# Kernel tuning notes

Measured on AMD Instinct MI355X. Metric: run time of the kernel, lower is better.

The kernel has to match this reference:

```python
import jax, jax.numpy as jnp
import numpy as np

MU = 5
ITERATIONS = 3


def _sobel(x):
    # torch kernel: stack([K, K.T]) with K = vertical-gradient Sobel; conv2d is cross-correlation
    k = jnp.array([[-1., -2., -1.], [0., 0., 0.], [1., 2., 1.]], dtype=x.dtype)
    kern = jnp.stack([k, k.T])[:, None]  # [2,1,3,3] -> channels (Gy, Gx)
    return jax.lax.conv_general_dilated(
        x, kern, window_strides=(1, 1), padding=[(1, 1), (1, 1)],
        dimension_numbers=("NCHW", "OIHW", "NCHW"))


def _normalize(v):
    # norm over channel dim, zeros replaced by 1 (matches tang_mag[tang_mag==0]=1)
    mag = jnp.linalg.norm(v, axis=1, keepdims=True)
    mag = jnp.where(mag == 0, jnp.ones_like(mag), mag)
    return v / mag


def etf_forward(inputs, mu=MU, iterations=ITERATIONS):
    B, _, H, W = inputs.shape
    sobel = _sobel(inputs)                                   # [B,2,H,W]
    sobel_mag = jnp.linalg.norm(sobel, axis=1, keepdims=True)
    sobel_mag = sobel_mag / jnp.max(sobel_mag)               # [B,1,H,W]
    pad = lambda t: jnp.pad(t, ((0, 0), (0, 0), (mu, mu), (mu, mu)))
    sobel_mag_padded = pad(sobel_mag)
    sobel_X = sobel_mag
    # tang = sobel.flip(channels) * [-1, 1] => [-Gx, Gy], then normalized
    tang = jnp.stack([-sobel[:, 1], sobel[:, 0]], axis=1)
    tang = _normalize(tang)
    for _ in range(iterations):
        for ori in ("Vertical", "Horizontal"):
            tang_padded = pad(tang)
            tang_X = tang
            acc = jnp.zeros_like(tang)
            for i in range(2 * mu + 1):
                if ori == "Vertical":
                    tang_Y = tang_padded[:, :, i:i + H, mu:mu + W]
                    sobel_Y = sobel_mag_padded[:, :, i:i + H, mu:mu + W]
                else:
                    tang_Y = tang_padded[:, :, mu:mu + H, i:i + W]
                    sobel_Y = sobel_mag_padded[:, :, mu:mu + H, i:i + W]
                w = (jnp.tanh(sobel_Y - sobel_X) + 1.0) * jnp.sum(tang_X * tang_Y, axis=1, keepdims=True) * 0.5
                acc = acc + tang_Y * w
            tang = _normalize(acc)
    return tang


def setup_inputs() -> dict:
    key = jax.random.key(0)
    inputs = jax.random.uniform(key, (2, 1, 1024, 1024), dtype=jnp.float32)
    return {"inputs": inputs}


def reference(inputs) -> jnp.ndarray:
    return etf_forward(inputs)
```

## Files before the change

### kernel.cpp

```cpp
#include <hip/hip_runtime.h>

#define BB 2
#define HH 1024
#define WW 1024
#define MU 5

#define TH 32
#define TW 64
#define SW (TW + 16)
#define SH (TH + 2 * MU)

__device__ __forceinline__ float fast_rcp(float x) { return __builtin_amdgcn_rcpf(x); }
__device__ __forceinline__ float fast_rsq(float x) { return __builtin_amdgcn_rsqf(x); }

#define SR 8
__global__ __launch_bounds__(256) void sobel_init(
    const float* __restrict__ x,
    float* __restrict__ tf,
    float* __restrict__ mag,
    float* __restrict__ block_max)
{
    __shared__ float xs[SR + 2][264];
    const int t = threadIdx.x;
    const int w0 = blockIdx.x * 256;
    const int h0 = blockIdx.y * SR;
    const int b = blockIdx.z;
    const size_t plane = (size_t)HH * WW;
    const float* xb = x + (size_t)b * plane;

    for (int i = t; i < (SR + 2) * 66; i += 256) {
        int r = i / 66, c4 = i % 66;
        int g = h0 - 1 + r;
        int gw = w0 - 4 + 4 * c4;
        float4 v = make_float4(0.f, 0.f, 0.f, 0.f);
        if (g >= 0 && g < HH && gw >= 0 && gw < WW)
            v = *(const float4*)(xb + (size_t)g * WW + gw);
        *(float4*)&xs[r][4 * c4] = v;
    }
    __syncthreads();

    float lmax = 0.f;
    const int c = 4 + t;
    #pragma unroll
    for (int k = 0; k < SR; ++k) {
        const float* rT = xs[k], * rM = xs[k + 1], * rB = xs[k + 2];
        float tl = rT[c - 1], tc = rT[c], tr = rT[c + 1];
        float ml = rM[c - 1],             mr = rM[c + 1];
        float bl = rB[c - 1], bc = rB[c], br = rB[c + 1];
        float s0 = (bl - tl) + 2.f * (bc - tc) + (br - tr);
        float s1 = (tr - tl) + 2.f * (mr - ml) + (br - bl);
        float m = sqrtf(fmaf(s0, s0, s1 * s1));
        float inv = (m == 0.f) ? 1.f : fast_rcp(m);
        size_t gi = (size_t)(h0 + k) * WW + (w0 + t);
        mag[(size_t)b * plane + gi] = m;
        ((float2*)tf)[(size_t)b * plane + gi] = make_float2(-s1 * inv, s0 * inv);
        lmax = fmaxf(lmax, m);
    }

    #pragma unroll
    for (int off = 32; off; off >>= 1) lmax = fmaxf(lmax, __shfl_down(lmax, off, 64));
    __shared__ float smax[4];
    if ((t & 63) == 0) smax[t >> 6] = lmax;
    __syncthreads();
    if (t == 0)
        block_max[(blockIdx.z * 128 + blockIdx.y) * 4 + blockIdx.x] =
            fmaxf(fmaxf(smax[0], smax[1]), fmaxf(smax[2], smax[3]));
}

__global__ __launch_bounds__(256) void reduce_max(
    const float* __restrict__ block_max, float* __restrict__ gmax)
{
    const int t = threadIdx.x;
    float m = 0.f;
    #pragma unroll
    for (int i = 0; i < 4; ++i) m = fmaxf(m, block_max[t + 256 * i]);
    #pragma unroll
    for (int off = 32; off; off >>= 1) m = fmaxf(m, __shfl_down(m, off, 64));
    __shared__ float smax[4];
    if ((t & 63) == 0) smax[t >> 6] = m;
    __syncthreads();
    if (t == 0) gmax[0] = fmaxf(fmaxf(smax[0], smax[1]), fmaxf(smax[2], smax[3]));
}

__global__ __launch_bounds__(256) void mag2em(
    float* __restrict__ mag, const float* __restrict__ gmax)
{
    const float s = 2.f * fast_rcp(gmax[0]);
    const int i = blockIdx.x * 256 + threadIdx.x;
    float4* p = (float4*)mag + i;
    float4 v = *p;
    v.x = __expf(-s * v.x);
    v.y = __expf(-s * v.y);
    v.z = __expf(-s * v.z);
    v.w = __expf(-s * v.w);
    *p = v;
}

template <int PLANAR_OUT>
__global__ __launch_bounds__(256) void etf_vh(
    const float* __restrict__ tin,
    float* __restrict__ tout,
    const float* __restrict__ em)
{
    __shared__ float lds[SH * SW * 3];
    float* st = lds;
    float* sm = lds + SH * SW * 2;
    float* sv = lds;

    const int t = threadIdx.x;
    const int w0 = blockIdx.x * TW;
    const int h0 = blockIdx.y * TH;
    const int b = blockIdx.z;
    const size_t plane = (size_t)HH * WW;
    const float* tb = tin + 2 * (size_t)b * plane;
    const float* mb = em + (size_t)b * plane;

    for (int i = t; i < SH * 40 + SH * 20; i += 256) {
        if (i < SH * 40) {
            int r = i / 40, c4 = i % 40;
            int g = h0 - MU + r;
            int gw = w0 - 8 + 2 * c4;
            float4 v = make_float4(0.f, 0.f, 0.f, 0.f);
            if (g >= 0 && g < HH && gw >= 0 && gw < WW)
                v = *(const float4*)(tb + 2 * ((size_t)g * WW + gw));
            *(float4*)&st[r * SW * 2 + 4 * c4] = v;
        } else {
            int j = i - SH * 40;
            int r = j / 20, c4 = j % 20;
            int g = h0 - MU + r;
            int gw = w0 - 8 + 4 * c4;
            float4 v = make_float4(1.f, 1.f, 1.f, 1.f);
            if (g >= 0 && g < HH && gw >= 0 && gw < WW)
                v = *(const float4*)(mb + (size_t)g * WW + gw);
            *(float4*)&sm[r * SW + 4 * c4] = v;
        }
    }
    __syncthreads();

    float vr0[10], vr1[10];
    #pragma unroll
    for (int k = 0; k < 10; ++k) {
        int px = t + 256 * k;
        int r = px / SW, c = px % SW;
        float2 tx = *(const float2*)&st[((r + MU) * SW + c) * 2];
        float remx = fast_rcp(sm[(r + MU) * SW + c]);
        float a0 = 0.f, a1 = 0.f;
        #pragma unroll
        for (int d = 0; d <= 2 * MU; ++d) {
            float2 ty = *(const float2*)&st[((r + d) * SW + c) * 2];
            float emy = sm[(r + d) * SW + c];
            float s = fast_rcp(fmaf(emy, remx, 1.f));
            float w = s * fmaf(tx.x, ty.x, tx.y * ty.y);
            a0 = fmaf(ty.x, w, a0);
            a1 = fmaf(ty.y, w, a1);
        }
        float n2 = fmaf(a0, a0, a1 * a1);
        float inv = (n2 == 0.f) ? 1.f : fast_rsq(n2);
        vr0[k] = a0 * inv;
        vr1[k] = a1 * inv;
    }
    __syncthreads();
    #pragma unroll
    for (int k = 0; k < 10; ++k) {
        int px = t + 256 * k;
        *(float2*)&sv[px * 2] = make_float2(vr0[k], vr1[k]);
    }
    __syncthreads();

    #pragma unroll
    for (int k = 0; k < 8; ++k) {
        int px = t + 256 * k;
        int r = px >> 6, c = px & 63;
        int sc = c + 8;
        float2 tx = *(const float2*)&sv[(r * SW + sc) * 2];
        float remx = fast_rcp(sm[(r + MU) * SW + sc]);
        float a0 = 0.f, a1 = 0.f;
        #pragma unroll
        for (int d = -MU; d <= MU; ++d) {
            float2 ty = *(const float2*)&sv[(r * SW + sc + d) * 2];
            float emy = sm[(r + MU) * SW + sc + d];
            float s = fast_rcp(fmaf(emy, remx, 1.f));
            float w = s * fmaf(tx.x, ty.x, tx.y * ty.y);
            a0 = fmaf(ty.x, w, a0);
            a1 = fmaf(ty.y, w, a1);
        }
        float n2 = fmaf(a0, a0, a1 * a1);
        float inv = (n2 == 0.f) ? 1.f : fast_rsq(n2);
        size_t gi = (size_t)(h0 + r) * WW + (w0 + c);
        if (PLANAR_OUT) {
            tout[(size_t)(2 * b)     * plane + gi] = a0 * inv;
            tout[(size_t)(2 * b + 1) * plane + gi] = a1 * inv;
        } else {
            *(float2*)&tout[2 * ((size_t)b * plane + gi)] = make_float2(a0 * inv, a1 * inv);
        }
    }
}

extern "C" void kernel_launch(void* const* d_in, const int* in_sizes, int n_in,
                              void* d_out, int out_size, void* d_ws, size_t ws_size,
                              hipStream_t stream)
{
    const float* x = (const float*)d_in[0];
    char* ws = (char*)d_ws;
    const size_t plane = (size_t)HH * WW;

    float* tfA  = (float*)ws;
    float* tfB  = (float*)(ws + sizeof(float) * BB * 2 * plane);
    float* mag  = (float*)(ws + sizeof(float) * BB * 4 * plane);
    float* gmax = (float*)(ws + sizeof(float) * BB * 6 * plane);
    float* block_max = gmax + 16;

    sobel_init<<<dim3(4, 128, BB), 256, 0, stream>>>(x, tfA, mag, block_max);
    reduce_max<<<1, 256, 0, stream>>>(block_max, gmax);
    mag2em<<<dim3(BB * plane / 1024), 256, 0, stream>>>(mag, gmax);

    dim3 g(WW / TW, HH / TH, BB);
    etf_vh<0><<<g, 256, 0, stream>>>(tfA, tfB, mag);
    etf_vh<0><<<g, 256, 0, stream>>>(tfB, tfA, mag);
    etf_vh<1><<<g, 256, 0, stream>>>(tfA, (float*)d_out, mag);
}
```

Before: 147.2 us.

## Split fused vertical-horizontal pass into register-sliding vertical and LDS horizontal kernels

Replaces the fused vertical+horizontal tile kernel, which recomputed vertical results on halo columns and staged them through LDS, with two separate kernels per iteration. The vertical kernel streams down a column strip and keeps a sliding register window of 18 rows. The horizontal kernel loads a 32x80 tile into padded LDS, and each thread keeps an 18-wide register window to produce 8 consecutive outputs. This removes the halo recompute and the LDS traffic of the fused version, at the cost of twice as many launches and an extra global round trip of the intermediate field per iteration.

```diff
diff --git a/kernel.cpp b/kernel.cpp
--- a/kernel.cpp
+++ b/kernel.cpp
@@ -5,18 +5,13 @@
 #define WW 1024
 #define MU 5
 
-#define TH 32
-#define TW 64
-#define SW (TW + 16)
-#define SH (TH + 2 * MU)
-
 __device__ __forceinline__ float fast_rcp(float x) { return __builtin_amdgcn_rcpf(x); }
 __device__ __forceinline__ float fast_rsq(float x) { return __builtin_amdgcn_rsqf(x); }
 
 #define SR 8
 __global__ __launch_bounds__(256) void sobel_init(
     const float* __restrict__ x,
-    float* __restrict__ tf,
+    float2* __restrict__ tf,
     float* __restrict__ mag,
     float* __restrict__ block_max)
 {
@@ -53,7 +48,7 @@
         float inv = (m == 0.f) ? 1.f : fast_rcp(m);
         size_t gi = (size_t)(h0 + k) * WW + (w0 + t);
         mag[(size_t)b * plane + gi] = m;
-        ((float2*)tf)[(size_t)b * plane + gi] = make_float2(-s1 * inv, s0 * inv);
+        tf[(size_t)b * plane + gi] = make_float2(-s1 * inv, s0 * inv);
         lmax = fmaxf(lmax, m);
     }
 
@@ -96,102 +91,117 @@
     *p = v;
 }
 
-template <int PLANAR_OUT>
-__global__ __launch_bounds__(256) void etf_vh(
-    const float* __restrict__ tin,
-    float* __restrict__ tout,
+#define VSTRIP 8
+__global__ __launch_bounds__(256) void etf_v(
+    const float2* __restrict__ tin, float2* __restrict__ tout,
     const float* __restrict__ em)
 {
-    __shared__ float lds[SH * SW * 3];
-    float* st = lds;
-    float* sm = lds + SH * SW * 2;
-    float* sv = lds;
-
-    const int t = threadIdx.x;
-    const int w0 = blockIdx.x * TW;
-    const int h0 = blockIdx.y * TH;
-    const int b = blockIdx.z;
-    const size_t plane = (size_t)HH * WW;
-    const float* tb = tin + 2 * (size_t)b * plane;
-    const float* mb = em + (size_t)b * plane;
-
-    for (int i = t; i < SH * 40 + SH * 20; i += 256) {
-        if (i < SH * 40) {
-            int r = i / 40, c4 = i % 40;
-            int g = h0 - MU + r;
-            int gw = w0 - 8 + 2 * c4;
-            float4 v = make_float4(0.f, 0.f, 0.f, 0.f);
-            if (g >= 0 && g < HH && gw >= 0 && gw < WW)
-                v = *(const float4*)(tb + 2 * ((size_t)g * WW + gw));
-            *(float4*)&st[r * SW * 2 + 4 * c4] = v;
-        } else {
-            int j = i - SH * 40;
-            int r = j / 20, c4 = j % 20;
-            int g = h0 - MU + r;
-            int gw = w0 - 8 + 4 * c4;
-            float4 v = make_float4(1.f, 1.f, 1.f, 1.f);
-            if (g >= 0 && g < HH && gw >= 0 && gw < WW)
-                v = *(const float4*)(mb + (size_t)g * WW + gw);
-            *(float4*)&sm[r * SW + 4 * c4] = v;
-        }
-    }
-    __syncthreads();
-
-    float vr0[10], vr1[10];
-    #pragma unroll
-    for (int k = 0; k < 10; ++k) {
-        int px = t + 256 * k;
-        int r = px / SW, c = px % SW;
-        float2 tx = *(const float2*)&st[((r + MU) * SW + c) * 2];
-        float remx = fast_rcp(sm[(r + MU) * SW + c]);
+    const int c  = blockIdx.x * 256 + threadIdx.x;
+    const int r0 = blockIdx.y * VSTRIP;
+    const int b  = blockIdx.z;
+    const size_t plane = (size_t)HH * WW;
+    const float2* tb = tin + (size_t)b * plane;
+    const float*  eb = em  + (size_t)b * plane;
+
+    float w0[VSTRIP + 10], w1[VSTRIP + 10], we[VSTRIP + 10];
+    #pragma unroll
+    for (int j = 0; j < 10; ++j) {
+        int g = r0 - MU + j;
+        float2 v = make_float2(0.f, 0.f); float e = 1.f;
+        if (g >= 0) { v = tb[(size_t)g * WW + c]; e = eb[(size_t)g * WW + c]; }
+        w0[j] = v.x; w1[j] = v.y; we[j] = e;
+    }
+    #pragma unroll
+    for (int i = 0; i < VSTRIP; ++i) {
+        int g = r0 + i + MU;
+        float2 v = make_float2(0.f, 0.f); float e = 1.f;
+        if (g < HH) { v = tb[(size_t)g * WW + c]; e = eb[(size_t)g * WW + c]; }
+        w0[i + 10] = v.x; w1[i + 10] = v.y; we[i + 10] = e;
+
+        float tx0 = w0[i + MU], tx1 = w1[i + MU];
+        float remx = fast_rcp(we[i + MU]);
         float a0 = 0.f, a1 = 0.f;
         #pragma unroll
         for (int d = 0; d <= 2 * MU; ++d) {
-            float2 ty = *(const float2*)&st[((r + d) * SW + c) * 2];
-            float emy = sm[(r + d) * SW + c];
-            float s = fast_rcp(fmaf(emy, remx, 1.f));
-            float w = s * fmaf(tx.x, ty.x, tx.y * ty.y);
-            a0 = fmaf(ty.x, w, a0);
-            a1 = fmaf(ty.y, w, a1);
+            float s = fast_rcp(fmaf(we[i + d], remx, 1.f));
+            float w = s * fmaf(tx0, w0[i + d], tx1 * w1[i + d]);
+            a0 = fmaf(w0[i + d], w, a0);
+            a1 = fmaf(w1[i + d], w, a1);
         }
         float n2 = fmaf(a0, a0, a1 * a1);
         float inv = (n2 == 0.f) ? 1.f : fast_rsq(n2);
-        vr0[k] = a0 * inv;
-        vr1[k] = a1 * inv;
-    }
-    __syncthreads();
-    #pragma unroll
-    for (int k = 0; k < 10; ++k) {
-        int px = t + 256 * k;
-        *(float2*)&sv[px * 2] = make_float2(vr0[k], vr1[k]);
-    }
-    __syncthreads();
+        tout[(size_t)b * plane + (size_t)(r0 + i) * WW + c] = make_float2(a0 * inv, a1 * inv);
+    }
+}
+
+template <int PLANAR_OUT>
+__global__ __launch_bounds__(256) void etf_h(
+    const float2* __restrict__ tin, float* __restrict__ tout,
+    const float* __restrict__ em)
+{
+    __shared__ float2 sT[32][81];
+    __shared__ float  sE[32][83];
+    const int t = threadIdx.x;
+    const int w0 = blockIdx.x * 64;
+    const int h0 = blockIdx.y * 32;
+    const int b = blockIdx.z;
+    const size_t plane = (size_t)HH * WW;
+    const float2* tb = tin + (size_t)b * plane;
+    const float*  eb = em  + (size_t)b * plane;
+
+    for (int i = t; i < 1920; i += 256) {
+        if (i < 1280) {
+            int r = i / 40, c4 = i % 40;
+            int gw = w0 - 8 + 2 * c4;
+            float4 v = make_float4(0.f, 0.f, 0.f, 0.f);
+            if (gw >= 0 && gw < WW)
+                v = *(const float4*)(tb + (size_t)(h0 + r) * WW + gw);
+            sT[r][c4 * 2]     = make_float2(v.x, v.y);
+            sT[r][c4 * 2 + 1] = make_float2(v.z, v.w);
+        } else {
+            int j = i - 1280;
+            int r = j / 20, c4 = j % 20;
+            int gw = w0 - 8 + 4 * c4;
+            float4 v = make_float4(1.f, 1.f, 1.f, 1.f);
+            if (gw >= 0 && gw < WW)
+                v = *(const float4*)(eb + (size_t)(h0 + r) * WW + gw);
+            sE[r][4 * c4] = v.x; sE[r][4 * c4 + 1] = v.y;
+            sE[r][4 * c4 + 2] = v.z; sE[r][4 * c4 + 3] = v.w;
+        }
+    }
+    __syncthreads();
+
+    const int r  = t & 31;
+    const int cg = t >> 5;
+    const int cb = 8 + cg * 8;
+    float h0a[18], h1a[18], hea[18];
+    #pragma unroll
+    for (int j = 0; j < 18; ++j) {
+        float2 v = sT[r][cb - MU + j];
+        h0a[j] = v.x; h1a[j] = v.y;
+        hea[j] = sE[r][cb - MU + j];
+    }
 
     #pragma unroll
     for (int k = 0; k < 8; ++k) {
-        int px = t + 256 * k;
-        int r = px >> 6, c = px & 63;
-        int sc = c + 8;
-        float2 tx = *(const float2*)&sv[(r * SW + sc) * 2];
-        float remx = fast_rcp(sm[(r + MU) * SW + sc]);
+        float tx0 = h0a[k + MU], tx1 = h1a[k + MU];
+        float remx = fast_rcp(hea[k + MU]);
         float a0 = 0.f, a1 = 0.f;
         #pragma unroll
-        for (int d = -MU; d <= MU; ++d) {
-            float2 ty = *(const float2*)&sv[(r * SW + sc + d) * 2];
-            float emy = sm[(r + MU) * SW + sc + d];
-            float s = fast_rcp(fmaf(emy, remx, 1.f));
-            float w = s * fmaf(tx.x, ty.x, tx.y * ty.y);
-            a0 = fmaf(ty.x, w, a0);
-            a1 = fmaf(ty.y, w, a1);
+        for (int d = 0; d <= 2 * MU; ++d) {
+            float s = fast_rcp(fmaf(hea[k + d], remx, 1.f));
+            float w = s * fmaf(tx0, h0a[k + d], tx1 * h1a[k + d]);
+            a0 = fmaf(h0a[k + d], w, a0);
+            a1 = fmaf(h1a[k + d], w, a1);
         }
         float n2 = fmaf(a0, a0, a1 * a1);
         float inv = (n2 == 0.f) ? 1.f : fast_rsq(n2);
-        size_t gi = (size_t)(h0 + r) * WW + (w0 + c);
+        size_t gi = (size_t)(h0 + r) * WW + (w0 + cg * 8 + k);
         if (PLANAR_OUT) {
             tout[(size_t)(2 * b)     * plane + gi] = a0 * inv;
             tout[(size_t)(2 * b + 1) * plane + gi] = a1 * inv;
         } else {
-            *(float2*)&tout[2 * ((size_t)b * plane + gi)] = make_float2(a0 * inv, a1 * inv);
+            ((float2*)tout)[(size_t)b * plane + gi] = make_float2(a0 * inv, a1 * inv);
         }
     }
 }
@@ -204,8 +214,8 @@
     char* ws = (char*)d_ws;
     const size_t plane = (size_t)HH * WW;
 
-    float* tfA  = (float*)ws;
-    float* tfB  = (float*)(ws + sizeof(float) * BB * 2 * plane);
+    float2* tfA = (float2*)ws;
+    float2* tfB = (float2*)(ws + sizeof(float) * BB * 2 * plane);
     float* mag  = (float*)(ws + sizeof(float) * BB * 4 * plane);
     float* gmax = (float*)(ws + sizeof(float) * BB * 6 * plane);
     float* block_max = gmax + 16;
@@ -214,8 +224,12 @@
     reduce_max<<<1, 256, 0, stream>>>(block_max, gmax);
     mag2em<<<dim3(BB * plane / 1024), 256, 0, stream>>>(mag, gmax);
 
-    dim3 g(WW / TW, HH / TH, BB);
-    etf_vh<0><<<g, 256, 0, stream>>>(tfA, tfB, mag);
-    etf_vh<0><<<g, 256, 0, stream>>>(tfB, tfA, mag);
-    etf_vh<1><<<g, 256, 0, stream>>>(tfA, (float*)d_out, mag);
-}
+    dim3 gv(4, HH / VSTRIP, BB);
+    dim3 gh(WW / 64, HH / 32, BB);
+    etf_v<<<gv, 256, 0, stream>>>(tfA, tfB, mag);
+    etf_h<0><<<gh, 256, 0, stream>>>(tfB, (float*)tfA, mag);
+    etf_v<<<gv, 256, 0, stream>>>(tfA, tfB, mag);
+    etf_h<0><<<gh, 256, 0, stream>>>(tfB, (float*)tfA, mag);
+    etf_v<<<gv, 256, 0, stream>>>(tfA, tfB, mag);
+    etf_h<1><<<gh, 256, 0, stream>>>(tfB, (float*)d_out, mag);
+}
```

Result: slower. 152.2 us (+3.4%).
